# Kernel optimization log

Measured on AMD Instinct MI355X. Metric: run time of the kernel, lower is better.

The kernel has to match this reference:

```python
import jax, jax.numpy as jnp
import numpy as np

N = 50000          # nodes
E = 1200000        # edges (before self loops)
HID = 256          # hidden_dim
HEADS = 4
DH = HID // HEADS  # head dim = 64
SLOPE = 0.2        # PyG GATConv default negative_slope


def setup_inputs() -> dict:
    key = jax.random.key(0)
    k1, k2, k3, k4, k5 = jax.random.split(key, 5)
    x = jax.random.normal(k1, (N, HID), dtype=jnp.float32)
    # GATConv params: shared linear W, per-head attention vectors a_src/a_dst, bias
    W = jax.random.normal(k2, (HID, HEADS * DH), dtype=jnp.float32) / np.float32(np.sqrt(HID))
    att_src = jax.random.normal(k3, (HEADS, DH), dtype=jnp.float32) * 0.1
    att_dst = jax.random.normal(k4, (HEADS, DH), dtype=jnp.float32) * 0.1
    bias = jnp.zeros((HEADS * DH,), dtype=jnp.float32)
    edge_index = jax.random.randint(k5, (2, E), 0, N, dtype=jnp.int32)
    return {"x": x, "W": W, "att_src": att_src, "att_dst": att_dst,
            "bias": bias, "edge_index": edge_index}


def reference(x, W, att_src, att_dst, bias, edge_index):
    # add self loops (PyG GATConv default add_self_loops=True)
    loops = jnp.arange(N, dtype=edge_index.dtype)
    src = jnp.concatenate([edge_index[0], loops])  # message source
    dst = jnpp_dst = jnp.concatenate([edge_index[1], loops])  # message target / softmax segment

    h = (x @ W).reshape(N, HEADS, DH)                       # [N,H,D]
    a_s = jnp.einsum('nhd,hd->nh', h, att_src)              # [N,H]
    a_d = jnp.einsum('nhd,hd->nh', h, att_dst)              # [N,H]

    e = jax.nn.leaky_relu(a_s[src] + a_d[dst], SLOPE)       # [Etot,H] edge logits
    # segment-wise (per destination node) stable softmax
    emax = jax.ops.segment_max(e, dst, num_segments=N)      # [N,H]
    ez = jnp.exp(e - emax[dst])
    denom = jax.ops.segment_sum(ez, dst, num_segments=N)    # [N,H]
    alpha = ez / (denom[dst] + 1e-16)                       # [Etot,H]

    msg = h[src] * alpha[:, :, None]                        # [Etot,H,D]
    out = jax.ops.segment_sum(msg, dst, num_segments=N)     # [N,H,D]
    out = out.reshape(N, HEADS * DH) + bias                 # concat heads + bias
    return jax.nn.relu(out)
```

## Files before the change

### kernel.cpp

```cpp
#include <hip/hip_runtime.h>
#include <hip/hip_bf16.h>
#include <hip/hip_fp16.h>

#define HID 256
#define HEADS 4
#define DH 64
#define SLOPE 0.2f
#define NBMAX 512
#define BCAP 4096

typedef __attribute__((ext_vector_type(8))) _Float16 f16x8;
typedef __attribute__((ext_vector_type(4))) float f32x4;

__device__ inline float leaky(float x) { return x >= 0.f ? x : SLOPE * x; }

__global__ __launch_bounds__(256) void transpose_w(const float* __restrict__ W,
                                                   _Float16* __restrict__ Wt) {
  int n = blockIdx.x;
  int k = threadIdx.x;
  Wt[n * HID + k] = (_Float16)W[(size_t)k * HID + n];
}

__global__ __launch_bounds__(512) void gemm_xw_f16(const float* __restrict__ X,
                                                   const _Float16* __restrict__ Wt,
                                                   const float* __restrict__ att_src,
                                                   const float* __restrict__ att_dst,
                                                   _Float16* __restrict__ Hp,
                                                   float* __restrict__ a_s,
                                                   float* __restrict__ a_d, int M) {
  __shared__ _Float16 sA[128][40];
  const int t = threadIdx.x;
  const int wave = t >> 6;
  const int l = t & 63;
  const int wm = wave >> 2;
  const int wn = wave & 3;
  const int row0 = blockIdx.x * 128;

  f32x4 acc[4][4] = {};

  for (int ks = 0; ks < 8; ++ks) {
    const int r = t >> 2;
    const int fo = (t & 3) * 8;
    const int gr = row0 + r;
    float4 v0 = make_float4(0.f, 0.f, 0.f, 0.f), v1 = v0;
    if (gr < M) {
      const float* p = X + (size_t)gr * HID + ks * 32 + fo;
      v0 = *(const float4*)p;
      v1 = *(const float4*)(p + 4);
    }
    _Float16 tmp[8] = {(_Float16)v0.x, (_Float16)v0.y, (_Float16)v0.z, (_Float16)v0.w,
                       (_Float16)v1.x, (_Float16)v1.y, (_Float16)v1.z, (_Float16)v1.w};
    __syncthreads();
    *(uint4*)&sA[r][fo] = *(uint4*)tmp;
    __syncthreads();

    f16x8 af[4];
#pragma unroll
    for (int mt = 0; mt < 4; ++mt)
      af[mt] = *(const f16x8*)&sA[wm * 64 + mt * 16 + (l & 15)][(l >> 4) * 8];
#pragma unroll
    for (int nt = 0; nt < 4; ++nt) {
      const f16x8 bfr = *(const f16x8*)(Wt + (size_t)(wn * 64 + nt * 16 + (l & 15)) * HID
                                        + ks * 32 + (l >> 4) * 8);
#pragma unroll
      for (int mt = 0; mt < 4; ++mt)
        acc[mt][nt] = __builtin_amdgcn_mfma_f32_16x16x32_f16(af[mt], bfr, acc[mt][nt], 0, 0, 0);
    }
  }

  const int head = wn;
  float as_v[4], ad_v[4];
#pragma unroll
  for (int nt = 0; nt < 4; ++nt) {
    as_v[nt] = att_src[head * DH + nt * 16 + (l & 15)];
    ad_v[nt] = att_dst[head * DH + nt * 16 + (l & 15)];
  }
#pragma unroll
  for (int mt = 0; mt < 4; ++mt) {
#pragma unroll
    for (int reg = 0; reg < 4; ++reg) {
      float ps = 0.f, pd = 0.f;
#pragma unroll
      for (int nt = 0; nt < 4; ++nt) {
        ps += acc[mt][nt][reg] * as_v[nt];
        pd += acc[mt][nt][reg] * ad_v[nt];
      }
#pragma unroll
      for (int off = 1; off < 16; off <<= 1) {
        ps += __shfl_xor(ps, off, 64);
        pd += __shfl_xor(pd, off, 64);
      }
      const int row = row0 + wm * 64 + mt * 16 + (l >> 4) * 4 + reg;
      if ((l & 15) == 0 && row < M) {
        a_s[(size_t)head * M + row] = ps;
        a_d[(size_t)head * M + row] = pd;
      }
    }
  }

#pragma unroll
  for (int mt = 0; mt < 4; ++mt) {
    const int rbase = row0 + wm * 64 + mt * 16 + (l >> 4) * 4;
#pragma unroll
    for (int nt = 0; nt < 4; ++nt) {
      const int dh = nt * 16 + (l & 15);
#pragma unroll
      for (int reg = 0; reg < 4; ++reg) {
        const int row = rbase + reg;
        if (row < M)
          Hp[((size_t)head * M + row) * DH + dh] = (_Float16)acc[mt][nt][reg];
      }
    }
  }
}

__global__ __launch_bounds__(256) void bucket_hist(const int* __restrict__ ei, int E, int Etot,
                                                   int* __restrict__ bucket_cnt, int NB) {
  __shared__ int h[NBMAX];
  for (int i = threadIdx.x; i < NB; i += 256) h[i] = 0;
  __syncthreads();
  const int g0 = blockIdx.x * 1024;
#pragma unroll
  for (int j = 0; j < 4; ++j) {
    const int e0 = (g0 + j * 256 + threadIdx.x) * 4;
    if (e0 >= Etot) continue;
    if (e0 >= E) {
#pragma unroll
      for (int k = 0; k < 4; ++k) atomicAdd(&h[(e0 - E + k) >> 7], 1);
    } else {
      const int4 d4 = *(const int4*)(ei + E + e0);
      atomicAdd(&h[d4.x >> 7], 1);
      atomicAdd(&h[d4.y >> 7], 1);
      atomicAdd(&h[d4.z >> 7], 1);
      atomicAdd(&h[d4.w >> 7], 1);
    }
  }
  __syncthreads();
  for (int i = threadIdx.x; i < NB; i += 256)
    if (h[i]) atomicAdd(&bucket_cnt[i], h[i]);
}

__global__ __launch_bounds__(512) void scan_buckets(const int* __restrict__ bucket_cnt,
                                                    int* __restrict__ bucket_base,
                                                    int* __restrict__ bucket_cursor,
                                                    int* __restrict__ offsets,
                                                    int Nn, int Etot, int NB) {
  __shared__ int h[512];
  const int tid = threadIdx.x;
  const int v = (tid < NB) ? bucket_cnt[tid] : 0;
  h[tid] = v;
  __syncthreads();
#pragma unroll
  for (int off = 1; off < 512; off <<= 1) {
    const int t = (tid >= off) ? h[tid - off] : 0;
    __syncthreads();
    h[tid] += t;
    __syncthreads();
  }
  if (tid < NB) {
    const int base = h[tid] - v;
    bucket_base[tid] = base;
    bucket_cursor[tid] = base;
  }
  if (tid == 0) offsets[Nn] = Etot;
}

__global__ __launch_bounds__(256) void scatter_tmp(const int* __restrict__ ei, int E, int Etot,
                                                   int* __restrict__ bucket_cursor,
                                                   unsigned* __restrict__ tmp, int NB) {
  __shared__ int h[NBMAX];
  __shared__ int cur[NBMAX];
  for (int i = threadIdx.x; i < NB; i += 256) h[i] = 0;
  __syncthreads();
  const int g0 = blockIdx.x * 1024;
#pragma unroll
  for (int j = 0; j < 4; ++j) {
    const int e0 = (g0 + j * 256 + threadIdx.x) * 4;
    if (e0 >= Etot) continue;
    if (e0 >= E) {
#pragma unroll
      for (int k = 0; k < 4; ++k) atomicAdd(&h[(e0 - E + k) >> 7], 1);
    } else {
      const int4 d4 = *(const int4*)(ei + E + e0);
      atomicAdd(&h[d4.x >> 7], 1);
      atomicAdd(&h[d4.y >> 7], 1);
      atomicAdd(&h[d4.z >> 7], 1);
      atomicAdd(&h[d4.w >> 7], 1);
    }
  }
  __syncthreads();
  for (int i = threadIdx.x; i < NB; i += 256)
    cur[i] = h[i] ? atomicAdd(&bucket_cursor[i], h[i]) : 0;
  __syncthreads();
#pragma unroll
  for (int j = 0; j < 4; ++j) {
    const int e0 = (g0 + j * 256 + threadIdx.x) * 4;
    if (e0 >= Etot) continue;
    int s[4], dn[4];
    if (e0 >= E) {
#pragma unroll
      for (int k = 0; k < 4; ++k) { s[k] = e0 - E + k; dn[k] = s[k]; }
    } else {
      const int4 s4 = *(const int4*)(ei + e0);
      const int4 d4 = *(const int4*)(ei + E + e0);
      s[0] = s4.x; s[1] = s4.y; s[2] = s4.z; s[3] = s4.w;
      dn[0] = d4.x; dn[1] = d4.y; dn[2] = d4.z; dn[3] = d4.w;
    }
#pragma unroll
    for (int k = 0; k < 4; ++k) {
      const int b = dn[k] >> 7;
      const int pos = atomicAdd(&cur[b], 1);
      tmp[pos] = (unsigned)s[k] | ((unsigned)(dn[k] & 127) << 16);
    }
  }
}

__global__ __launch_bounds__(256) void csr_build(const unsigned* __restrict__ tmp,
                                                 const int* __restrict__ bucket_base,
                                                 const int* __restrict__ bucket_cursor,
                                                 int* __restrict__ offsets,
                                                 int* __restrict__ csr_src, int Nn) {
  __shared__ int h[128], cur[128];
  __shared__ int cs[BCAP];
  const int b = blockIdx.x;
  const int start = bucket_base[b];
  const int cnt = min(bucket_cursor[b] - start, BCAP);
  const int tid = threadIdx.x;
  if (tid < 128) h[tid] = 0;
  __syncthreads();
  for (int i = tid; i < cnt; i += 256)
    atomicAdd(&h[tmp[start + i] >> 16], 1);
  __syncthreads();
  const int own = (tid < 128) ? h[tid] : 0;
#pragma unroll
  for (int off = 1; off < 128; off <<= 1) {
    const int t = (tid < 128 && tid >= off) ? h[tid - off] : 0;
    __syncthreads();
    if (tid < 128) h[tid] += t;
    __syncthreads();
  }
  if (tid < 128) {
    const int excl = h[tid] - own;
    cur[tid] = excl;
    const int n = b * 128 + tid;
    if (n < Nn) offsets[n] = start + excl;
  }
  __syncthreads();
  for (int i = tid; i < cnt; i += 256) {
    const unsigned p = tmp[start + i];
    const int pos = atomicAdd(&cur[p >> 16], 1);
    cs[pos] = (int)(p & 0xffffu);
  }
  __syncthreads();
  for (int i = tid; i < cnt; i += 256)
    csr_src[start + i] = cs[i];
}

__global__ __launch_bounds__(256) void gat_agg2(const int* __restrict__ offsets,
                                                const int* __restrict__ csr_src,
                                                const float* __restrict__ a_s,
                                                const float* __restrict__ a_d,
                                                const _Float16* __restrict__ Hp,
                                                const float* __restrict__ bias,
                                                float* __restrict__ out, int Nn, int nbNode) {
  const int head = blockIdx.x / nbNode;
  const int nb   = blockIdx.x - head * nbNode;
  const int wave = threadIdx.x >> 6;
  const int lane = threadIdx.x & 63;
  const int half = lane >> 5;
  const int hl   = lane & 31;
  const int g2   = hl >> 3;
  const int sl   = hl & 7;
  const int n    = nb * 8 + wave * 2 + half;

  int start = 0, end = 0;
  if (n < Nn) { start = offsets[n]; end = offsets[n + 1]; }
  const float* __restrict__ as_h = a_s + (size_t)head * Nn;
  const float adn = (n < Nn) ? a_d[(size_t)head * Nn + n] : 0.f;
  const _Float16* __restrict__ Hh = Hp + (size_t)head * Nn * DH + sl * 8;

  float m = -INFINITY, l = 0.f;
  __half2 acc[4];
#pragma unroll
  for (int j = 0; j < 4; ++j) acc[j] = __float2half2_rn(0.f);

  const int nChunk = (end - start + 31) >> 5;
  for (int c = 0; c < nChunk; ++c) {
    const int base = start + c * 32;
    const int cnt = min(32, end - base);
    const int idx = min(base + hl, end - 1);
    const int src = csr_src[idx];
    const float lg = leaky(as_h[src] + adn);
    const float logit = (hl < cnt) ? lg : -INFINITY;

    float cm = logit;
#pragma unroll
    for (int off = 16; off > 0; off >>= 1) cm = fmaxf(cm, __shfl_xor(cm, off, 64));
    const float nm = fmaxf(m, cm);
    const float scale = __expf(m - nm);
    const __half2 s2 = __float2half2_rn(scale);
#pragma unroll
    for (int j = 0; j < 4; ++j) acc[j] = __hmul2(acc[j], s2);
    l *= scale;
    const float p = __expf(logit - nm);
    float psum = p;
#pragma unroll
    for (int off = 16; off > 0; off >>= 1) psum += __shfl_xor(psum, off, 64);
    l += psum;
    m = nm;

    const unsigned combo = (unsigned)src |
                           ((unsigned)__half_as_ushort(__float2half(p)) << 16);
    const int nIt = (cnt + 3) >> 2;
    for (int i = 0; i < nIt; ++i) {
      const int e = i * 4 + g2;
      const unsigned cc = (unsigned)__shfl((int)combo, half * 32 + e, 64);
      const unsigned se = cc & 0xffffu;
      const __half ah = __ushort_as_half((unsigned short)(cc >> 16));
      const __half2 a2 = __halves2half2(ah, ah);
      const uint4 hv = *(const uint4*)(Hh + (size_t)se * DH);
      acc[0] = __hfma2(a2, *(const __half2*)&hv.x, acc[0]);
      acc[1] = __hfma2(a2, *(const __half2*)&hv.y, acc[1]);
      acc[2] = __hfma2(a2, *(const __half2*)&hv.z, acc[2]);
      acc[3] = __hfma2(a2, *(const __half2*)&hv.w, acc[3]);
    }
  }
#pragma unroll
  for (int off = 8; off <= 16; off <<= 1)
#pragma unroll
    for (int j = 0; j < 4; ++j) {
      int tbits = __shfl_xor(*(const int*)&acc[j], off, 64);
      acc[j] = __hadd2(acc[j], *(const __half2*)&tbits);
    }

  if (hl < 8 && n < Nn) {
    const float inv = 1.f / (l + 1e-16f);
    float v[8];
#pragma unroll
    for (int j = 0; j < 4; ++j) {
      v[2 * j]     = __low2float(acc[j]);
      v[2 * j + 1] = __high2float(acc[j]);
    }
#pragma unroll
    for (int j = 0; j < 8; ++j)
      v[j] = fmaxf(v[j] * inv + bias[head * DH + sl * 8 + j], 0.f);
    float* op = out + (size_t)n * HID + head * DH + sl * 8;
    *(float4*)op = make_float4(v[0], v[1], v[2], v[3]);
    *(float4*)(op + 4) = make_float4(v[4], v[5], v[6], v[7]);
  }
}

extern "C" void kernel_launch(void* const* d_in, const int* in_sizes, int n_in,
                              void* d_out, int out_size, void* d_ws, size_t ws_size,
                              hipStream_t stream) {
  const float* x       = (const float*)d_in[0];
  const float* Wm      = (const float*)d_in[1];
  const float* att_src = (const float*)d_in[2];
  const float* att_dst = (const float*)d_in[3];
  const float* bias    = (const float*)d_in[4];
  const int*   ei      = (const int*)d_in[5];

  const int Nn   = in_sizes[0] / HID;
  const int E    = in_sizes[5] / 2;
  const int Etot = E + Nn;
  const int NB   = (Nn + 127) >> 7;

  float* out = (float*)d_out;

  _Float16* Hp    = (_Float16*)d_ws;
  _Float16* Wt    = Hp + (size_t)HEADS * Nn * DH;
  float* a_s      = (float*)(Wt + HID * HID);
  float* a_d      = a_s + (size_t)HEADS * Nn;
  int*   offsets  = (int*)(a_d + (size_t)HEADS * Nn);
  int*   bucket_cnt    = offsets + (Nn + 1);
  int*   bucket_base   = bucket_cnt + NBMAX;
  int*   bucket_cursor = bucket_base + NBMAX;
  unsigned* tmp   = (unsigned*)(bucket_cursor + NBMAX);
  int*   csr_src  = (int*)(tmp + Etot);

  const int nbNode = (Nn + 7) / 8;
  const int nbEdge = (Etot + 4095) / 4096;

  hipMemsetAsync(bucket_cnt, 0, NBMAX * sizeof(int), stream);

  transpose_w<<<HID, HID, 0, stream>>>(Wm, Wt);
  gemm_xw_f16<<<(Nn + 127) / 128, 512, 0, stream>>>(x, Wt, att_src, att_dst,
                                                    Hp, a_s, a_d, Nn);

  bucket_hist<<<nbEdge, 256, 0, stream>>>(ei, E, Etot, bucket_cnt, NB);
  scan_buckets<<<1, 512, 0, stream>>>(bucket_cnt, bucket_base, bucket_cursor,
                                      offsets, Nn, Etot, NB);
  scatter_tmp<<<nbEdge, 256, 0, stream>>>(ei, E, Etot, bucket_cursor, tmp, NB);
  csr_build<<<NB, 256, 0, stream>>>(tmp, bucket_base, bucket_cursor,
                                    offsets, csr_src, Nn);
  gat_agg2<<<HEADS * nbNode, 256, 0, stream>>>(offsets, csr_src, a_s, a_d, Hp, bias,
                                               out, Nn, nbNode);
}
```

Baseline: 182.9 us.

## Replace per-node aggregation with per-bucket shared-memory softmax and accumulation

Replaces the per-node online-softmax aggregation kernel with a per-bucket kernel: each block handles 128 destination nodes for one head. It computes the segment max and denominator via shared-memory atomics, then splits the edge range evenly across 32 lane-groups that accumulate half-precision partial sums and flush them into a shared fp32 accumulator with atomics. The CSR build now writes packed src/dst-local entries directly instead of staging through shared memory and emitting per-node offsets. The memset is folded into the transpose kernel. This is meant to remove load imbalance and per-node offset handling, at the cost of three passes over the edges and many shared atomics. The grid is also much smaller (4 × 391 blocks), which may reduce occupancy.

```diff
diff --git a/kernel.cpp b/kernel.cpp
--- a/kernel.cpp
+++ b/kernel.cpp
@@ -7,18 +7,30 @@
 #define DH 64
 #define SLOPE 0.2f
 #define NBMAX 512
-#define BCAP 4096
 
 typedef __attribute__((ext_vector_type(8))) _Float16 f16x8;
 typedef __attribute__((ext_vector_type(4))) float f32x4;
 
 __device__ inline float leaky(float x) { return x >= 0.f ? x : SLOPE * x; }
+__device__ inline unsigned enc_f(float f) {
+  unsigned u = __float_as_uint(f);
+  return (u & 0x80000000u) ? ~u : (u | 0x80000000u);
+}
+__device__ inline float dec_f(unsigned u) {
+  unsigned v = (u & 0x80000000u) ? (u & 0x7fffffffu) : ~u;
+  return __uint_as_float(v);
+}
 
 __global__ __launch_bounds__(256) void transpose_w(const float* __restrict__ W,
-                                                   _Float16* __restrict__ Wt) {
+                                                   _Float16* __restrict__ Wt,
+                                                   int* __restrict__ bucket_cnt) {
   int n = blockIdx.x;
   int k = threadIdx.x;
   Wt[n * HID + k] = (_Float16)W[(size_t)k * HID + n];
+  if (n == 0) {
+    bucket_cnt[k] = 0;
+    bucket_cnt[k + 256] = 0;
+  }
 }
 
 __global__ __launch_bounds__(512) void gemm_xw_f16(const float* __restrict__ X,
@@ -142,9 +154,7 @@
 
 __global__ __launch_bounds__(512) void scan_buckets(const int* __restrict__ bucket_cnt,
                                                     int* __restrict__ bucket_base,
-                                                    int* __restrict__ bucket_cursor,
-                                                    int* __restrict__ offsets,
-                                                    int Nn, int Etot, int NB) {
+                                                    int* __restrict__ bucket_cursor, int NB) {
   __shared__ int h[512];
   const int tid = threadIdx.x;
   const int v = (tid < NB) ? bucket_cnt[tid] : 0;
@@ -162,7 +172,6 @@
     bucket_base[tid] = base;
     bucket_cursor[tid] = base;
   }
-  if (tid == 0) offsets[Nn] = Etot;
 }
 
 __global__ __launch_bounds__(256) void scatter_tmp(const int* __restrict__ ei, int E, int Etot,
@@ -218,13 +227,11 @@
 __global__ __launch_bounds__(256) void csr_build(const unsigned* __restrict__ tmp,
                                                  const int* __restrict__ bucket_base,
                                                  const int* __restrict__ bucket_cursor,
-                                                 int* __restrict__ offsets,
-                                                 int* __restrict__ csr_src, int Nn) {
+                                                 unsigned* __restrict__ csr) {
   __shared__ int h[128], cur[128];
-  __shared__ int cs[BCAP];
   const int b = blockIdx.x;
   const int start = bucket_base[b];
-  const int cnt = min(bucket_cursor[b] - start, BCAP);
+  const int cnt = bucket_cursor[b] - start;
   const int tid = threadIdx.x;
   if (tid < 128) h[tid] = 0;
   __syncthreads();
@@ -239,114 +246,137 @@
     if (tid < 128) h[tid] += t;
     __syncthreads();
   }
-  if (tid < 128) {
-    const int excl = h[tid] - own;
-    cur[tid] = excl;
-    const int n = b * 128 + tid;
-    if (n < Nn) offsets[n] = start + excl;
-  }
+  if (tid < 128) cur[tid] = h[tid] - own;
   __syncthreads();
   for (int i = tid; i < cnt; i += 256) {
     const unsigned p = tmp[start + i];
     const int pos = atomicAdd(&cur[p >> 16], 1);
-    cs[pos] = (int)(p & 0xffffu);
-  }
-  __syncthreads();
-  for (int i = tid; i < cnt; i += 256)
-    csr_src[start + i] = cs[i];
-}
-
-__global__ __launch_bounds__(256) void gat_agg2(const int* __restrict__ offsets,
-                                                const int* __restrict__ csr_src,
-                                                const float* __restrict__ a_s,
-                                                const float* __restrict__ a_d,
-                                                const _Float16* __restrict__ Hp,
-                                                const float* __restrict__ bias,
-                                                float* __restrict__ out, int Nn, int nbNode) {
-  const int head = blockIdx.x / nbNode;
-  const int nb   = blockIdx.x - head * nbNode;
-  const int wave = threadIdx.x >> 6;
-  const int lane = threadIdx.x & 63;
-  const int half = lane >> 5;
-  const int hl   = lane & 31;
-  const int g2   = hl >> 3;
-  const int sl   = hl & 7;
-  const int n    = nb * 8 + wave * 2 + half;
-
-  int start = 0, end = 0;
-  if (n < Nn) { start = offsets[n]; end = offsets[n + 1]; }
+    csr[start + pos] = p;
+  }
+}
+
+__global__ __launch_bounds__(256) void gat_bucket(const unsigned* __restrict__ csr,
+                                                  const int* __restrict__ bucket_base,
+                                                  const int* __restrict__ bucket_cursor,
+                                                  const float* __restrict__ a_s,
+                                                  const float* __restrict__ a_d,
+                                                  const _Float16* __restrict__ Hp,
+                                                  const float* __restrict__ bias,
+                                                  float* __restrict__ out, int Nn, int NB) {
+  __shared__ float accL[128][DH];
+  __shared__ float adL[128];
+  __shared__ unsigned mEnc[128];
+  __shared__ float mL[128];
+  __shared__ float lL[128];
+
+  const int head = blockIdx.x / NB;
+  const int b    = blockIdx.x - head * NB;
+  const int tid  = threadIdx.x;
+  const int start = bucket_base[b];
+  const int cnt   = bucket_cursor[b] - start;
+  const unsigned* __restrict__ ecsr = csr + start;
   const float* __restrict__ as_h = a_s + (size_t)head * Nn;
-  const float adn = (n < Nn) ? a_d[(size_t)head * Nn + n] : 0.f;
-  const _Float16* __restrict__ Hh = Hp + (size_t)head * Nn * DH + sl * 8;
-
-  float m = -INFINITY, l = 0.f;
-  __half2 acc[4];
-#pragma unroll
-  for (int j = 0; j < 4; ++j) acc[j] = __float2half2_rn(0.f);
-
-  const int nChunk = (end - start + 31) >> 5;
-  for (int c = 0; c < nChunk; ++c) {
-    const int base = start + c * 32;
-    const int cnt = min(32, end - base);
-    const int idx = min(base + hl, end - 1);
-    const int src = csr_src[idx];
-    const float lg = leaky(as_h[src] + adn);
-    const float logit = (hl < cnt) ? lg : -INFINITY;
-
-    float cm = logit;
-#pragma unroll
-    for (int off = 16; off > 0; off >>= 1) cm = fmaxf(cm, __shfl_xor(cm, off, 64));
-    const float nm = fmaxf(m, cm);
-    const float scale = __expf(m - nm);
-    const __half2 s2 = __float2half2_rn(scale);
-#pragma unroll
-    for (int j = 0; j < 4; ++j) acc[j] = __hmul2(acc[j], s2);
-    l *= scale;
-    const float p = __expf(logit - nm);
-    float psum = p;
-#pragma unroll
-    for (int off = 16; off > 0; off >>= 1) psum += __shfl_xor(psum, off, 64);
-    l += psum;
-    m = nm;
-
-    const unsigned combo = (unsigned)src |
-                           ((unsigned)__half_as_ushort(__float2half(p)) << 16);
-    const int nIt = (cnt + 3) >> 2;
-    for (int i = 0; i < nIt; ++i) {
-      const int e = i * 4 + g2;
-      const unsigned cc = (unsigned)__shfl((int)combo, half * 32 + e, 64);
-      const unsigned se = cc & 0xffffu;
-      const __half ah = __ushort_as_half((unsigned short)(cc >> 16));
-      const __half2 a2 = __halves2half2(ah, ah);
-      const uint4 hv = *(const uint4*)(Hh + (size_t)se * DH);
-      acc[0] = __hfma2(a2, *(const __half2*)&hv.x, acc[0]);
-      acc[1] = __hfma2(a2, *(const __half2*)&hv.y, acc[1]);
-      acc[2] = __hfma2(a2, *(const __half2*)&hv.z, acc[2]);
-      acc[3] = __hfma2(a2, *(const __half2*)&hv.w, acc[3]);
-    }
-  }
-#pragma unroll
-  for (int off = 8; off <= 16; off <<= 1)
-#pragma unroll
-    for (int j = 0; j < 4; ++j) {
-      int tbits = __shfl_xor(*(const int*)&acc[j], off, 64);
-      acc[j] = __hadd2(acc[j], *(const __half2*)&tbits);
-    }
-
-  if (hl < 8 && n < Nn) {
-    const float inv = 1.f / (l + 1e-16f);
-    float v[8];
-#pragma unroll
-    for (int j = 0; j < 4; ++j) {
-      v[2 * j]     = __low2float(acc[j]);
-      v[2 * j + 1] = __high2float(acc[j]);
-    }
-#pragma unroll
-    for (int j = 0; j < 8; ++j)
-      v[j] = fmaxf(v[j] * inv + bias[head * DH + sl * 8 + j], 0.f);
-    float* op = out + (size_t)n * HID + head * DH + sl * 8;
-    *(float4*)op = make_float4(v[0], v[1], v[2], v[3]);
-    *(float4*)(op + 4) = make_float4(v[4], v[5], v[6], v[7]);
+  const _Float16* __restrict__ Hph = Hp + (size_t)head * Nn * DH;
+
+  {
+    float4 z = make_float4(0.f, 0.f, 0.f, 0.f);
+    float* ap = &accL[tid >> 1][(tid & 1) * 32];
+#pragma unroll
+    for (int j = 0; j < 8; ++j) *(float4*)(ap + j * 4) = z;
+    if (tid < 128) {
+      const int n = b * 128 + tid;
+      adL[tid] = (n < Nn) ? a_d[(size_t)head * Nn + n] : 0.f;
+      mEnc[tid] = enc_f(-INFINITY);
+      lL[tid] = 0.f;
+    }
+  }
+  __syncthreads();
+
+  for (int i = tid; i < cnt; i += 256) {
+    const unsigned p = ecsr[i];
+    const int dnl = p >> 16;
+    const float logit = leaky(as_h[p & 0xffffu] + adL[dnl]);
+    atomicMax(&mEnc[dnl], enc_f(logit));
+  }
+  __syncthreads();
+  if (tid < 128) mL[tid] = dec_f(mEnc[tid]);
+  __syncthreads();
+
+  for (int i = tid; i < cnt; i += 256) {
+    const unsigned p = ecsr[i];
+    const int dnl = p >> 16;
+    const float logit = leaky(as_h[p & 0xffffu] + adL[dnl]);
+    atomicAdd(&lL[dnl], __expf(logit - mL[dnl]));
+  }
+  __syncthreads();
+  if (tid < 128) lL[tid] = 1.f / (lL[tid] + 1e-16f);
+  __syncthreads();
+
+  {
+    const int sg = tid >> 3;
+    const int sl = tid & 7;
+    const int len = (cnt + 31) >> 5;
+    const int i0 = sg * len;
+    const int i1 = min(i0 + len, cnt);
+    int prev = -1;
+    __half2 racc[4];
+#pragma unroll
+    for (int j = 0; j < 4; ++j) racc[j] = __float2half2_rn(0.f);
+
+    for (int i = i0; i < i1; ++i) {
+      const unsigned p = ecsr[i];
+      const int src = p & 0xffffu;
+      const int dnl = p >> 16;
+      if (dnl != prev) {
+        if (prev >= 0) {
+#pragma unroll
+          for (int j = 0; j < 4; ++j) {
+            const float2 f = __half22float2(racc[j]);
+            atomicAdd(&accL[prev][sl * 8 + 2 * j], f.x);
+            atomicAdd(&accL[prev][sl * 8 + 2 * j + 1], f.y);
+            racc[j] = __float2half2_rn(0.f);
+          }
+        }
+        prev = dnl;
+      }
+      const float logit = leaky(as_h[src] + adL[dnl]);
+      const float alpha = __expf(logit - mL[dnl]) * lL[dnl];
+      const __half2 a2 = __float2half2_rn(alpha);
+      const uint4 hv = *(const uint4*)(Hph + (size_t)src * DH + sl * 8);
+      racc[0] = __hfma2(a2, *(const __half2*)&hv.x, racc[0]);
+      racc[1] = __hfma2(a2, *(const __half2*)&hv.y, racc[1]);
+      racc[2] = __hfma2(a2, *(const __half2*)&hv.z, racc[2]);
+      racc[3] = __hfma2(a2, *(const __half2*)&hv.w, racc[3]);
+    }
+    if (prev >= 0) {
+#pragma unroll
+      for (int j = 0; j < 4; ++j) {
+        const float2 f = __half22float2(racc[j]);
+        atomicAdd(&accL[prev][sl * 8 + 2 * j], f.x);
+        atomicAdd(&accL[prev][sl * 8 + 2 * j + 1], f.y);
+      }
+    }
+  }
+  __syncthreads();
+
+  {
+    const int node = tid >> 1;
+    const int d0 = (tid & 1) * 32;
+    const int n = b * 128 + node;
+    if (n < Nn) {
+      float* op = out + (size_t)n * HID + head * DH + d0;
+      const float* bp = bias + head * DH + d0;
+#pragma unroll
+      for (int k = 0; k < 8; ++k) {
+        float4 v = *(const float4*)(&accL[node][d0 + k * 4]);
+        const float4 bb = *(const float4*)(bp + k * 4);
+        v.x = fmaxf(v.x + bb.x, 0.f);
+        v.y = fmaxf(v.y + bb.y, 0.f);
+        v.z = fmaxf(v.z + bb.z, 0.f);
+        v.w = fmaxf(v.w + bb.w, 0.f);
+        *(float4*)(op + k * 4) = v;
+      }
+    }
   }
 }
 
@@ -371,28 +401,22 @@
   _Float16* Wt    = Hp + (size_t)HEADS * Nn * DH;
   float* a_s      = (float*)(Wt + HID * HID);
   float* a_d      = a_s + (size_t)HEADS * Nn;
-  int*   offsets  = (int*)(a_d + (size_t)HEADS * Nn);
-  int*   bucket_cnt    = offsets + (Nn + 1);
+  int*   bucket_cnt    = (int*)(a_d + (size_t)HEADS * Nn);
   int*   bucket_base   = bucket_cnt + NBMAX;
   int*   bucket_cursor = bucket_base + NBMAX;
   unsigned* tmp   = (unsigned*)(bucket_cursor + NBMAX);
-  int*   csr_src  = (int*)(tmp + Etot);
-
-  const int nbNode = (Nn + 7) / 8;
+  unsigned* csr   = tmp + Etot;
+
   const int nbEdge = (Etot + 4095) / 4096;
 
-  hipMemsetAsync(bucket_cnt, 0, NBMAX * sizeof(int), stream);
-
-  transpose_w<<<HID, HID, 0, stream>>>(Wm, Wt);
+  transpose_w<<<HID, HID, 0, stream>>>(Wm, Wt, bucket_cnt);
   gemm_xw_f16<<<(Nn + 127) / 128, 512, 0, stream>>>(x, Wt, att_src, att_dst,
                                                     Hp, a_s, a_d, Nn);
 
   bucket_hist<<<nbEdge, 256, 0, stream>>>(ei, E, Etot, bucket_cnt, NB);
-  scan_buckets<<<1, 512, 0, stream>>>(bucket_cnt, bucket_base, bucket_cursor,
-                                      offsets, Nn, Etot, NB);
+  scan_buckets<<<1, 512, 0, stream>>>(bucket_cnt, bucket_base, bucket_cursor, NB);
   scatter_tmp<<<nbEdge, 256, 0, stream>>>(ei, E, Etot, bucket_cursor, tmp, NB);
-  csr_build<<<NB, 256, 0, stream>>>(tmp, bucket_base, bucket_cursor,
-                                    offsets, csr_src, Nn);
-  gat_agg2<<<HEADS * nbNode, 256, 0, stream>>>(offsets, csr_src, a_s, a_d, Hp, bias,
-                                               out, Nn, nbNode);
-}
+  csr_build<<<NB, 256, 0, stream>>>(tmp, bucket_base, bucket_cursor, csr);
+  gat_bucket<<<HEADS * NB, 256, 0, stream>>>(csr, bucket_base, bucket_cursor,
+                                             a_s, a_d, Hp, bias, out, Nn, NB);
+}
```

After: 313.0 us. +71.1%, slower.
